# Performance work log

Measured on AMD Instinct MI355X. Metric: run time of the kernel, lower is better.

The kernel has to match this reference:

```python
import jax, jax.numpy as jnp
import numpy as np

B, D, K, NDIM = 4, 81, 2048, 4  # batch, feature dim, n mixture components, box coord dims


def setup_inputs() -> dict:
    key = jax.random.key(0)
    k1, k2, k3, k4 = jax.random.split(key, 4)
    x = jax.random.normal(k1, (B, D, K), dtype=jnp.float32)
    # mixture weights, positive and normalized over components
    pi = jax.nn.softmax(jax.random.normal(k2, (B, 1, K), dtype=jnp.float32), axis=2)
    # component means in [0,1] (normalized box coords)
    mu = jax.random.uniform(k3, (B, NDIM, K), dtype=jnp.float32)
    # positive scales
    sig = jax.random.uniform(k4, (B, NDIM, K), dtype=jnp.float32) * 0.1 + 0.01
    return {"x": x, "pi": pi, "mu": mu, "sig": sig}


def _cauchy_pdf(mu, sig, points):
    # mu, sig: (B, 1, NDIM, K); points: (B, P, NDIM, 1)
    d = points - mu
    return sig / (jnp.pi * (d * d + sig * sig))


def reference(x, pi, mu, sig):
    # points = mu.transpose(1,2): evaluate the mixture at each component mean
    points = jnp.transpose(mu, (0, 2, 1))            # (B, K, NDIM)
    comp = _cauchy_pdf(mu[:, None, :, :], sig[:, None, :, :],
                       points[:, :, :, None])        # (B, K, NDIM, K)
    comp = jnp.prod(comp, axis=2)                    # independent dims -> (B, K, K)
    lh = pi * comp                                   # pi (B,1,K) broadcasts over points
    coef = lh / jnp.sum(lh, axis=2, keepdims=True)   # normalize over components
    coef = jax.lax.stop_gradient(coef)               # coef_detach=True
    y = jnp.einsum('bdk,bkm->bdm', x, coef)          # torch.bmm(x, coef)
    return y
```

## Files before the change

kernel.cpp:

```cpp
#include <hip/hip_runtime.h>


typedef float v4f __attribute__((ext_vector_type(4)));
typedef float f32x4 __attribute__((ext_vector_type(4)));
typedef short bf16x8 __attribute__((ext_vector_type(8)));

namespace {
constexpr int BB = 4;
constexpr int DD = 81;
constexpr int KK = 2048;
constexpr int MROWS = 96;
constexpr float INV_PI4 = 1.0f / 97.40909103400243f;

constexpr size_t OFF_XBF = 0;
constexpr size_t OFF_RSP = (size_t)BB * MROWS * KK * 2;
}

__device__ __forceinline__ unsigned short f2bf(float f) {
    union { float f; unsigned int u; } v; v.f = f;
    unsigned int u = v.u;
    unsigned int r = (u + 0x7FFFu + ((u >> 16) & 1u)) >> 16;
    return (unsigned short)r;
}

__global__ __launch_bounds__(256) void rowsum_kernel(const float* __restrict__ pi_,
                                                     const float* __restrict__ mu,
                                                     const float* __restrict__ sig,
                                                     float* __restrict__ rowsumPart) {
    __shared__ v4f   mush[256];
    __shared__ v4f   s2sh[256];
    __shared__ float csh[256];
    __shared__ float red[4][64];

    int blk = blockIdx.x;
    int b   = blk >> 8;
    int pc  = (blk & 255) >> 3;
    int ms  = blk & 7;
    int p0  = pc * 64;
    int m0  = ms * 256;
    int t   = threadIdx.x;
    int lane = t & 63, w = t >> 6;

    const float* mub = mu  + (size_t)b * 4 * KK;
    const float* sgb = sig + (size_t)b * 4 * KK;
    const float* pib = pi_ + (size_t)b * KK;

    {
        int m = m0 + t;
        v4f mm = {mub[m], mub[KK + m], mub[2 * KK + m], mub[3 * KK + m]};
        v4f sg = {sgb[m], sgb[KK + m], sgb[2 * KK + m], sgb[3 * KK + m]};
        mush[t] = mm;
        s2sh[t] = sg * sg;
        csh[t]  = pib[m] * ((sg.x * sg.y) * (sg.z * sg.w)) * INV_PI4;
    }
    int p = p0 + lane;
    v4f mp = {mub[p], mub[KK + p], mub[2 * KK + p], mub[3 * KK + p]};
    __syncthreads();

    float sum = 0.f;
#pragma unroll 4
    for (int i = 0; i < 64; ++i) {
        int mi = w * 64 + i;
        v4f d = mp - mush[mi];
        v4f q = d * d + s2sh[mi];
        float den = (q.x * q.y) * (q.z * q.w);
        sum += csh[mi] * __builtin_amdgcn_rcpf(den);
    }

    red[w][lane] = sum;
    __syncthreads();
    if (t < 64)
        rowsumPart[((size_t)(b * 8 + ms)) * KK + p0 + t] =
            red[0][t] + red[1][t] + red[2][t] + red[3][t];
}

__global__ __launch_bounds__(256) void xbf_kernel(const float* __restrict__ x,
                                                  const float* __restrict__ rowsumPart,
                                                  unsigned short* __restrict__ xbf) {
    int d = blockIdx.x;
    int b = blockIdx.y;
    int t = threadIdx.x;
    unsigned short* orow = xbf + ((size_t)(b * MROWS + d)) * KK;
    const float* xrow = x + ((size_t)(b * DD + d)) * KK;
    const float* rsp  = rowsumPart + (size_t)b * 8 * KK;
#pragma unroll
    for (int j = 0; j < 8; ++j) {
        int p = j * 256 + t;
        float rs = 0.f;
#pragma unroll
        for (int s = 0; s < 8; ++s) rs += rsp[(size_t)s * KK + p];
        float v = 0.f;
        if (d < DD) v = xrow[p] * __builtin_amdgcn_rcpf(rs);
        orow[p] = f2bf(v);
    }
}

__global__ __launch_bounds__(512) void gemm_kernel(const float* __restrict__ pi_,
                                                   const float* __restrict__ mu,
                                                   const float* __restrict__ sig,
                                                   const unsigned short* __restrict__ xbf,
                                                   float* __restrict__ out) {
    __shared__ __align__(16) char smem[49152];
    v4f* mus = (v4f*)smem;
    f32x4 (*red)[6][64] = (f32x4 (*)[6][64])smem;

    int t = threadIdx.x;
    int w = t >> 6, lane = t & 63;
    int r = lane & 15, q = lane >> 4;
    int b  = blockIdx.y;
    int m0 = blockIdx.x * 16;

    const float* mub = mu  + (size_t)b * 4 * KK;
    const float* sgb = sig + (size_t)b * 4 * KK;

    for (int i = t; i < KK; i += 512)
        mus[i] = (v4f){mub[i], mub[KK + i], mub[2 * KK + i], mub[3 * KK + i]};

    int m = m0 + r;
    v4f mm = {mub[m], mub[KK + m], mub[2 * KK + m], mub[3 * KK + m]};
    v4f sg = {sgb[m], sgb[KK + m], sgb[2 * KK + m], sgb[3 * KK + m]};
    v4f s2 = sg * sg;
    float cm = pi_[(size_t)b * KK + m] * ((sg.x * sg.y) * (sg.z * sg.w)) * INV_PI4;

    const unsigned short* Abase = xbf + ((size_t)(b * MROWS + r)) * KK;

    f32x4 acc[6];
#pragma unroll
    for (int i = 0; i < 6; ++i) acc[i] = (f32x4)0.f;

    __syncthreads();

    int pw = w * 256;
#pragma unroll
    for (int ks = 0; ks < 8; ++ks) {
        int pb = pw + ks * 32 + q * 8;
        bf16x8 Bf;
#pragma unroll
        for (int j = 0; j < 8; ++j) {
            v4f mp = mus[pb + j];
            v4f dd = mp - mm;
            v4f qq = dd * dd + s2;
            float den = (qq.x * qq.y) * (qq.z * qq.w);
            float lh = cm * __builtin_amdgcn_rcpf(den);
            Bf[j] = (short)f2bf(lh);
        }
        bf16x8 Af[6];
#pragma unroll
        for (int Mt = 0; Mt < 6; ++Mt)
            Af[Mt] = *(const bf16x8*)(Abase + (size_t)Mt * 16 * KK + pb);
#pragma unroll
        for (int Mt = 0; Mt < 6; ++Mt)
            acc[Mt] = __builtin_amdgcn_mfma_f32_16x16x32_bf16(Af[Mt], Bf, acc[Mt], 0, 0, 0);
    }

    __syncthreads();
#pragma unroll
    for (int Mt = 0; Mt < 6; ++Mt)
        red[w][Mt][lane] = acc[Mt];
    __syncthreads();

    int col = t & 15;
    int dr  = t >> 4;
#pragma unroll
    for (int k = 0; k < 3; ++k) {
        int d = dr + 32 * k;
        if (d < DD) {
            int Mt  = d >> 4;
            int row = d & 15;
            int l   = (row >> 2) * 16 + col;
            int j   = row & 3;
            float s = 0.f;
#pragma unroll
            for (int ww = 0; ww < 8; ++ww) s += red[ww][Mt][l][j];
            out[((size_t)(b * DD + d)) * KK + m0 + col] = s;
        }
    }
}

extern "C" void kernel_launch(void* const* d_in, const int* in_sizes, int n_in,
                              void* d_out, int out_size, void* d_ws, size_t ws_size,
                              hipStream_t stream) {
    const float* x   = (const float*)d_in[0];
    const float* pi_ = (const float*)d_in[1];
    const float* mu  = (const float*)d_in[2];
    const float* sig = (const float*)d_in[3];
    float* out = (float*)d_out;

    unsigned short* xbf = (unsigned short*)((char*)d_ws + OFF_XBF);
    float* rowsumPart   = (float*)((char*)d_ws + OFF_RSP);

    rowsum_kernel<<<1024, 256, 0, stream>>>(pi_, mu, sig, rowsumPart);
    dim3 xg(MROWS, BB);
    xbf_kernel<<<xg, 256, 0, stream>>>(x, rowsumPart, xbf);
    dim3 gg(KK / 16, BB);
    gemm_kernel<<<gg, 512, 0, stream>>>(pi_, mu, sig, xbf, out);
}
```

Measured before the change: 100.7 us.

## Fuse x conversion into rowsum kernel and widen GEMM tile to 32 columns

Removes the separate xbf kernel: the prep kernel now converts x to bf16 alongside the row-sum computation, and the 1/rowsum scaling moves into the GEMM's B-fragment generation through a shared-memory table of inverse sums. The GEMM block now covers 32 output columns with two accumulator sets, so each A fragment load feeds two MFMAs, at the cost of more registers and half as many blocks. This drops one launch and one dependent pass over x, but each GEMM block now re-reduces all 8 partial row sums.

```diff
diff --git a/kernel.cpp b/kernel.cpp
--- a/kernel.cpp
+++ b/kernel.cpp
@@ -23,10 +23,12 @@
     return (unsigned short)r;
 }
 
-__global__ __launch_bounds__(256) void rowsum_kernel(const float* __restrict__ pi_,
-                                                     const float* __restrict__ mu,
-                                                     const float* __restrict__ sig,
-                                                     float* __restrict__ rowsumPart) {
+__global__ __launch_bounds__(256) void prep_kernel(const float* __restrict__ x,
+                                                   const float* __restrict__ pi_,
+                                                   const float* __restrict__ mu,
+                                                   const float* __restrict__ sig,
+                                                   float* __restrict__ rowsumPart,
+                                                   unsigned short* __restrict__ xbf) {
     __shared__ v4f   mush[256];
     __shared__ v4f   s2sh[256];
     __shared__ float csh[256];
@@ -55,6 +57,20 @@
     }
     int p = p0 + lane;
     v4f mp = {mub[p], mub[KK + p], mub[2 * KK + p], mub[3 * KK + p]};
+
+    {
+        int rembase = (blk & 255) * 768;
+        const float* xb = x + (size_t)b * DD * KK;
+#pragma unroll
+        for (int k = 0; k < 3; ++k) {
+            int rem = rembase + k * 256 + t;
+            int d   = rem >> 11;
+            int pp  = rem & 2047;
+            float v = 0.f;
+            if (d < DD) v = xb[(size_t)d * KK + pp];
+            xbf[(size_t)b * MROWS * KK + rem] = f2bf(v);
+        }
+    }
     __syncthreads();
 
     float sum = 0.f;
@@ -74,59 +90,51 @@
             red[0][t] + red[1][t] + red[2][t] + red[3][t];
 }
 
-__global__ __launch_bounds__(256) void xbf_kernel(const float* __restrict__ x,
-                                                  const float* __restrict__ rowsumPart,
-                                                  unsigned short* __restrict__ xbf) {
-    int d = blockIdx.x;
-    int b = blockIdx.y;
-    int t = threadIdx.x;
-    unsigned short* orow = xbf + ((size_t)(b * MROWS + d)) * KK;
-    const float* xrow = x + ((size_t)(b * DD + d)) * KK;
-    const float* rsp  = rowsumPart + (size_t)b * 8 * KK;
-#pragma unroll
-    for (int j = 0; j < 8; ++j) {
-        int p = j * 256 + t;
-        float rs = 0.f;
-#pragma unroll
-        for (int s = 0; s < 8; ++s) rs += rsp[(size_t)s * KK + p];
-        float v = 0.f;
-        if (d < DD) v = xrow[p] * __builtin_amdgcn_rcpf(rs);
-        orow[p] = f2bf(v);
-    }
-}
-
 __global__ __launch_bounds__(512) void gemm_kernel(const float* __restrict__ pi_,
                                                    const float* __restrict__ mu,
                                                    const float* __restrict__ sig,
+                                                   const float* __restrict__ rowsumPart,
                                                    const unsigned short* __restrict__ xbf,
                                                    float* __restrict__ out) {
     __shared__ __align__(16) char smem[49152];
-    v4f* mus = (v4f*)smem;
+    v4f*   mus  = (v4f*)smem;
+    float* invs = (float*)(smem + 32768);
     f32x4 (*red)[6][64] = (f32x4 (*)[6][64])smem;
 
     int t = threadIdx.x;
     int w = t >> 6, lane = t & 63;
     int r = lane & 15, q = lane >> 4;
     int b  = blockIdx.y;
-    int m0 = blockIdx.x * 16;
+    int m0 = blockIdx.x * 32;
 
     const float* mub = mu  + (size_t)b * 4 * KK;
     const float* sgb = sig + (size_t)b * 4 * KK;
+    const float* rspb = rowsumPart + (size_t)b * 8 * KK;
 
     for (int i = t; i < KK; i += 512)
         mus[i] = (v4f){mub[i], mub[KK + i], mub[2 * KK + i], mub[3 * KK + i]};
-
-    int m = m0 + r;
-    v4f mm = {mub[m], mub[KK + m], mub[2 * KK + m], mub[3 * KK + m]};
-    v4f sg = {sgb[m], sgb[KK + m], sgb[2 * KK + m], sgb[3 * KK + m]};
-    v4f s2 = sg * sg;
-    float cm = pi_[(size_t)b * KK + m] * ((sg.x * sg.y) * (sg.z * sg.w)) * INV_PI4;
+    for (int i = t; i < KK; i += 512) {
+        float s = 0.f;
+#pragma unroll
+        for (int sidx = 0; sidx < 8; ++sidx) s += rspb[(size_t)sidx * KK + i];
+        invs[i] = __builtin_amdgcn_rcpf(s);
+    }
+
+    int mA = m0 + r, mB = m0 + 16 + r;
+    v4f mmA = {mub[mA], mub[KK + mA], mub[2 * KK + mA], mub[3 * KK + mA]};
+    v4f sgA = {sgb[mA], sgb[KK + mA], sgb[2 * KK + mA], sgb[3 * KK + mA]};
+    v4f s2A = sgA * sgA;
+    float cA = pi_[(size_t)b * KK + mA] * ((sgA.x * sgA.y) * (sgA.z * sgA.w)) * INV_PI4;
+    v4f mmB = {mub[mB], mub[KK + mB], mub[2 * KK + mB], mub[3 * KK + mB]};
+    v4f sgB = {sgb[mB], sgb[KK + mB], sgb[2 * KK + mB], sgb[3 * KK + mB]};
+    v4f s2B = sgB * sgB;
+    float cB = pi_[(size_t)b * KK + mB] * ((sgB.x * sgB.y) * (sgB.z * sgB.w)) * INV_PI4;
 
     const unsigned short* Abase = xbf + ((size_t)(b * MROWS + r)) * KK;
 
-    f32x4 acc[6];
-#pragma unroll
-    for (int i = 0; i < 6; ++i) acc[i] = (f32x4)0.f;
+    f32x4 acc0[6], acc1[6];
+#pragma unroll
+    for (int i = 0; i < 6; ++i) { acc0[i] = (f32x4)0.f; acc1[i] = (f32x4)0.f; }
 
     __syncthreads();
 
@@ -134,45 +142,53 @@
 #pragma unroll
     for (int ks = 0; ks < 8; ++ks) {
         int pb = pw + ks * 32 + q * 8;
-        bf16x8 Bf;
+        bf16x8 Bf0, Bf1;
 #pragma unroll
         for (int j = 0; j < 8; ++j) {
-            v4f mp = mus[pb + j];
-            v4f dd = mp - mm;
-            v4f qq = dd * dd + s2;
-            float den = (qq.x * qq.y) * (qq.z * qq.w);
-            float lh = cm * __builtin_amdgcn_rcpf(den);
-            Bf[j] = (short)f2bf(lh);
+            v4f mp  = mus[pb + j];
+            float iv = invs[pb + j];
+            v4f d0 = mp - mmA;
+            v4f q0 = d0 * d0 + s2A;
+            float den0 = (q0.x * q0.y) * (q0.z * q0.w);
+            Bf0[j] = (short)f2bf((cA * iv) * __builtin_amdgcn_rcpf(den0));
+            v4f d1 = mp - mmB;
+            v4f q1 = d1 * d1 + s2B;
+            float den1 = (q1.x * q1.y) * (q1.z * q1.w);
+            Bf1[j] = (short)f2bf((cB * iv) * __builtin_amdgcn_rcpf(den1));
         }
         bf16x8 Af[6];
 #pragma unroll
         for (int Mt = 0; Mt < 6; ++Mt)
             Af[Mt] = *(const bf16x8*)(Abase + (size_t)Mt * 16 * KK + pb);
 #pragma unroll
-        for (int Mt = 0; Mt < 6; ++Mt)
-            acc[Mt] = __builtin_amdgcn_mfma_f32_16x16x32_bf16(Af[Mt], Bf, acc[Mt], 0, 0, 0);
-    }
-
-    __syncthreads();
-#pragma unroll
-    for (int Mt = 0; Mt < 6; ++Mt)
-        red[w][Mt][lane] = acc[Mt];
-    __syncthreads();
+        for (int Mt = 0; Mt < 6; ++Mt) {
+            acc0[Mt] = __builtin_amdgcn_mfma_f32_16x16x32_bf16(Af[Mt], Bf0, acc0[Mt], 0, 0, 0);
+            acc1[Mt] = __builtin_amdgcn_mfma_f32_16x16x32_bf16(Af[Mt], Bf1, acc1[Mt], 0, 0, 0);
+        }
+    }
 
     int col = t & 15;
     int dr  = t >> 4;
 #pragma unroll
-    for (int k = 0; k < 3; ++k) {
-        int d = dr + 32 * k;
-        if (d < DD) {
-            int Mt  = d >> 4;
-            int row = d & 15;
-            int l   = (row >> 2) * 16 + col;
-            int j   = row & 3;
-            float s = 0.f;
-#pragma unroll
-            for (int ww = 0; ww < 8; ++ww) s += red[ww][Mt][l][j];
-            out[((size_t)(b * DD + d)) * KK + m0 + col] = s;
+    for (int nt = 0; nt < 2; ++nt) {
+        __syncthreads();
+#pragma unroll
+        for (int Mt = 0; Mt < 6; ++Mt)
+            red[w][Mt][lane] = (nt == 0) ? acc0[Mt] : acc1[Mt];
+        __syncthreads();
+#pragma unroll
+        for (int k = 0; k < 3; ++k) {
+            int d = dr + 32 * k;
+            if (d < DD) {
+                int Mt  = d >> 4;
+                int row = d & 15;
+                int l   = (row >> 2) * 16 + col;
+                int j   = row & 3;
+                float s = 0.f;
+#pragma unroll
+                for (int ww = 0; ww < 8; ++ww) s += red[ww][Mt][l][j];
+                out[((size_t)(b * DD + d)) * KK + m0 + nt * 16 + col] = s;
+            }
         }
     }
 }
@@ -189,9 +205,7 @@
     unsigned short* xbf = (unsigned short*)((char*)d_ws + OFF_XBF);
     float* rowsumPart   = (float*)((char*)d_ws + OFF_RSP);
 
-    rowsum_kernel<<<1024, 256, 0, stream>>>(pi_, mu, sig, rowsumPart);
-    dim3 xg(MROWS, BB);
-    xbf_kernel<<<xg, 256, 0, stream>>>(x, rowsumPart, xbf);
-    dim3 gg(KK / 16, BB);
-    gemm_kernel<<<gg, 512, 0, stream>>>(pi_, mu, sig, xbf, out);
-}
+    prep_kernel<<<1024, 256, 0, stream>>>(x, pi_, mu, sig, rowsumPart, xbf);
+    dim3 gg(KK / 32, BB);
+    gemm_kernel<<<gg, 512, 0, stream>>>(pi_, mu, sig, rowsumPart, xbf, out);
+}
```

Result: faster. 92.08 us (-8.6%).
